# Kernel optimization log

Measured on AMD Instinct MI355X. Metric: run time of the kernel, lower is better.

Reference implementation:

```python
import math
import jax, jax.numpy as jnp
import numpy as np

B, T, S = 2, 2048, 2048
D_MODEL, N_HEADS = 1024, 16
HEAD_DIM = D_MODEL // N_HEADS
OUT_DIM = 1024


def setup_inputs() -> dict:
    key = jax.random.key(0)
    ks = jax.random.split(key, 6)
    q = jax.random.normal(ks[0], (B, T, D_MODEL), dtype=jnp.float32)
    k = jax.random.normal(ks[1], (B, S, D_MODEL), dtype=jnp.float32)
    v = jax.random.normal(ks[2], (B, S, D_MODEL), dtype=jnp.float32)
    rel_pos_bias = jax.random.normal(ks[3], (T, S, N_HEADS), dtype=jnp.float32)
    # shared qkv projection weight (torch ModuleList([Linear]*3) aliases one module)
    lim = 1.0 / math.sqrt(D_MODEL)
    Wqkv = jax.random.uniform(ks[4], (D_MODEL, D_MODEL), minval=-lim, maxval=lim, dtype=jnp.float32)
    Wout = jax.random.uniform(ks[5], (OUT_DIM, D_MODEL), minval=-lim, maxval=lim, dtype=jnp.float32)
    logit_scale = jnp.full((N_HEADS, 1, 1), math.log(10.0), dtype=jnp.float32)
    return {"q": q, "k": k, "v": v, "rel_pos_bias": rel_pos_bias,
            "Wqkv": Wqkv, "Wout": Wout, "logit_scale": logit_scale}


def _l2norm(x, eps=1e-12):
    # matches torch F.normalize(dim=-1)
    n = jnp.sqrt(jnp.sum(x * x, axis=-1, keepdims=True))
    return x / jnp.maximum(n, eps)


def reference(q, k, v, rel_pos_bias, Wqkv, Wout, logit_scale):
    # shared qkv projection (Linear, no bias): x @ W.T
    qp = q @ Wqkv.T
    kp = k @ Wqkv.T
    vp = v @ Wqkv.T
    # [B, H, T, Dh]
    qh = qp.reshape(B, T, N_HEADS, HEAD_DIM).transpose(0, 2, 1, 3)
    kh = kp.reshape(B, S, N_HEADS, HEAD_DIM).transpose(0, 2, 1, 3)
    vh = vp.reshape(B, S, N_HEADS, HEAD_DIM).transpose(0, 2, 1, 3)
    # cosine attention with clamped learned logit scale
    scale = jnp.exp(jnp.minimum(logit_scale, math.log(100.0)))  # [H,1,1]
    attn = jnp.einsum('bhtd,bhsd->bhts', _l2norm(qh), _l2norm(kh)) * scale
    # rel_pos_bias [T,S,H] -> [H,T,S], broadcast over batch
    attn = attn + rel_pos_bias.transpose(2, 0, 1)
    attn = jax.nn.softmax(attn, axis=-1)
    vals = jnp.einsum('bhts,bhsd->bhtd', attn, vh)
    vals = vals.transpose(0, 2, 1, 3).reshape(B, T, D_MODEL)
    return vals @ Wout.T
```

## Files before the change

### kernel.cpp

```cpp
#include <hip/hip_runtime.h>
#include <stdint.h>

typedef unsigned short u16;
using bf16x8 = __attribute__((ext_vector_type(8))) __bf16;
using f32x4  = __attribute__((ext_vector_type(4))) float;
using u16x8  = __attribute__((ext_vector_type(8))) u16;

#define BB 2
#define TT 2048
#define SQ 2048
#define DM 1024
#define NH 16
#define HD 64

__device__ __forceinline__ float bf2f(u16 u) {
  uint32_t x = ((uint32_t)u) << 16;
  return __builtin_bit_cast(float, x);
}
__device__ __forceinline__ u16 f2bf(float f) {
  uint32_t x = __builtin_bit_cast(uint32_t, f);
  x += 0x7fffu + ((x >> 16) & 1u);
  return (u16)(x >> 16);
}

typedef __attribute__((address_space(1))) void gvoid;
typedef __attribute__((address_space(3))) void lvoid;
__device__ __forceinline__ void g2l16(const void* g, void* l) {
  __builtin_amdgcn_global_load_lds((gvoid*)g, (lvoid*)l, 16, 0, 0);
}

__global__ __launch_bounds__(256) void convert_f32_bf16(
    const float* __restrict__ src, u16* __restrict__ dst, int n8) {
  int i = blockIdx.x * 256 + threadIdx.x;
  if (i >= n8) return;
  f32x4 a = ((const f32x4*)src)[(size_t)i * 2];
  f32x4 b = ((const f32x4*)src)[(size_t)i * 2 + 1];
  u16x8 o;
#pragma unroll
  for (int j = 0; j < 4; ++j) { o[j] = f2bf(a[j]); o[4 + j] = f2bf(b[j]); }
  ((u16x8*)dst)[i] = o;
}

template <typename OutT>
__device__ __forceinline__ void gemm_body(const u16* __restrict__ A,
                                          const u16* __restrict__ W,
                                          OutT* __restrict__ C,
                                          const float* __restrict__ ls,
                                          int norm_mode) {
  const int n0 = blockIdx.x * 128;
  const int m0 = blockIdx.y * 128;
  const int tid = threadIdx.x;
  const int w = tid >> 6, lane = tid & 63;
  const int l15 = lane & 15, lg = lane >> 4;
  const int wr = w >> 1, wc = w & 1;

  __shared__ u16 ldsA[16 * 512];
  __shared__ u16 ldsB[16 * 512];

  f32x4 acc[4][4];
#pragma unroll
  for (int i = 0; i < 4; ++i)
#pragma unroll
    for (int j = 0; j < 4; ++j) acc[i][j] = (f32x4){0.f, 0.f, 0.f, 0.f};

  for (int kt = 0; kt < 1024; kt += 64) {
#pragma unroll
    for (int u = 0; u < 4; ++u) {
      int f = w * 4 + u;
      int mt = f >> 1, ks = f & 1;
      g2l16(A + (size_t)(m0 + mt * 16 + l15) * 1024 + kt + ks * 32 + lg * 8,
            &ldsA[f * 512]);
      g2l16(W + (size_t)(n0 + mt * 16 + l15) * 1024 + kt + ks * 32 + lg * 8,
            &ldsB[f * 512]);
    }
    __syncthreads();
#pragma unroll
    for (int ks = 0; ks < 2; ++ks) {
      bf16x8 a[4], b[4];
#pragma unroll
      for (int i = 0; i < 4; ++i)
        a[i] = *(const bf16x8*)&ldsA[((wr * 4 + i) * 2 + ks) * 512 + lane * 8];
#pragma unroll
      for (int j = 0; j < 4; ++j)
        b[j] = *(const bf16x8*)&ldsB[((wc * 4 + j) * 2 + ks) * 512 + lane * 8];
#pragma unroll
      for (int i = 0; i < 4; ++i)
#pragma unroll
        for (int j = 0; j < 4; ++j)
          acc[i][j] = __builtin_amdgcn_mfma_f32_16x16x32_bf16(a[i], b[j],
                                                              acc[i][j], 0, 0, 0);
    }
    __syncthreads();
  }

  if (norm_mode < 2) {
    float sc = 1.0f;
    if (norm_mode == 0) sc = __expf(fminf(ls[(n0 >> 6) + wc], 4.60517019f));
#pragma unroll
    for (int i = 0; i < 4; ++i)
#pragma unroll
      for (int r = 0; r < 4; ++r) {
        float ss = 0.f;
#pragma unroll
        for (int j = 0; j < 4; ++j) ss += acc[i][j][r] * acc[i][j][r];
#pragma unroll
        for (int d = 1; d < 16; d <<= 1) ss += __shfl_xor(ss, d, 64);
        float f = sc / fmaxf(sqrtf(ss), 1e-12f);
#pragma unroll
        for (int j = 0; j < 4; ++j) acc[i][j][r] *= f;
      }
  }

#pragma unroll
  for (int i = 0; i < 4; ++i) {
    int row0 = m0 + (wr * 4 + i) * 16 + lg * 4;
#pragma unroll
    for (int j = 0; j < 4; ++j) {
      int col = n0 + (wc * 4 + j) * 16 + l15;
#pragma unroll
      for (int r = 0; r < 4; ++r) {
        if constexpr (sizeof(OutT) == 2)
          C[(size_t)(row0 + r) * 1024 + col] = f2bf(acc[i][j][r]);
        else
          C[(size_t)(row0 + r) * 1024 + col] = acc[i][j][r];
      }
    }
  }
}

__global__ __launch_bounds__(256, 2) void gemm_qkv(
    const u16* __restrict__ q, const u16* __restrict__ k,
    const u16* __restrict__ v, const u16* __restrict__ W,
    const float* __restrict__ ls,
    u16* __restrict__ qp, u16* __restrict__ kp, u16* __restrict__ vp) {
  const u16* A;
  u16* C;
  if (blockIdx.z == 0) { A = q; C = qp; }
  else if (blockIdx.z == 1) { A = k; C = kp; }
  else { A = v; C = vp; }
  gemm_body<u16>(A, W, C, ls, blockIdx.z);
}

__global__ __launch_bounds__(256, 2) void gemm_out(const u16* __restrict__ A,
                                                   const u16* __restrict__ W,
                                                   float* __restrict__ C) {
  gemm_body<float>(A, W, C, nullptr, 2);
}

__global__ __launch_bounds__(256) void transpose_v(const u16* __restrict__ vp,
                                                   u16* __restrict__ vt) {
  int st = blockIdx.x;
  int bh = blockIdx.y;
  __shared__ u16 lds[64][72];
  int tid = threadIdx.x;
  int s = tid >> 2, c0 = (tid & 3) * 16;
  int b = bh >> 4, h = bh & 15;
  const u16* src = vp + (size_t)(b * SQ + st * 64 + s) * 1024 + h * 64 + c0;
  u16x8 r0 = *(const u16x8*)src;
  u16x8 r1 = *(const u16x8*)(src + 8);
#pragma unroll
  for (int j = 0; j < 8; ++j) { lds[s][c0 + j] = r0[j]; lds[s][c0 + 8 + j] = r1[j]; }
  __syncthreads();
  int d = tid >> 2, sc = (tid & 3) * 16;
  u16x8 o0, o1;
#pragma unroll
  for (int j = 0; j < 8; ++j) { o0[j] = lds[sc + j][d]; o1[j] = lds[sc + 8 + j][d]; }
  u16* dst = vt + (size_t)(bh * 64 + d) * SQ + st * 64 + sc;
  *(u16x8*)dst = o0;
  *((u16x8*)(dst + 8)) = o1;
}

__global__ __launch_bounds__(256) void transpose_bias(const float* __restrict__ bias,
                                                      u16* __restrict__ bt) {
  int t = blockIdx.y;
  int s0 = blockIdx.x * 512;
  __shared__ u16 lds[16][520];
  int tid = threadIdx.x;
  const float* src = bias + ((size_t)t * SQ + s0 + tid * 2) * 16;
  float v[32];
#pragma unroll
  for (int j = 0; j < 8; ++j) {
    f32x4 r = ((const f32x4*)src)[j];
#pragma unroll
    for (int e = 0; e < 4; ++e) v[j * 4 + e] = r[e];
  }
  int sl = tid * 2;
#pragma unroll
  for (int e = 0; e < 32; ++e) lds[e & 15][sl + (e >> 4)] = f2bf(v[e]);
  __syncthreads();
  int h = tid >> 4, sc = (tid & 15) * 32;
  u16* dst = bt + ((size_t)h * TT + t) * SQ + s0 + sc;
#pragma unroll
  for (int j = 0; j < 4; ++j) {
    u16x8 o;
#pragma unroll
    for (int e = 0; e < 8; ++e) o[e] = lds[h][sc + j * 8 + e];
    *((u16x8*)(dst + j * 8)) = o;
  }
}

__global__ __launch_bounds__(256, 2) void flash_attn(
    const u16* __restrict__ qn, const u16* __restrict__ kn,
    const u16* __restrict__ vt, const u16* __restrict__ bt,
    u16* __restrict__ av) {
  const int h = blockIdx.x >> 1, b = blockIdx.x & 1, qt = blockIdx.y;
  const int tid = threadIdx.x, w = tid >> 6, lane = tid & 63;
  const int l15 = lane & 15, lg = lane >> 4;

  __shared__ u16 ldsK[16 * 512];
  __shared__ u16 ldsV[16 * 512];
  __shared__ u16 ldsP[4][16 * 136];

  const int t0 = qt * 64 + w * 16;

  bf16x8 qf[2];
  {
    const u16* qb = qn + (size_t)(b * TT + t0 + l15) * 1024 + h * 64 + lg * 8;
    qf[0] = *(const bf16x8*)qb;
    qf[1] = *(const bf16x8*)(qb + 32);
  }

  f32x4 o[4];
  float li[4];
#pragma unroll
  for (int r = 0; r < 4; ++r) li[r] = 0.f;
#pragma unroll
  for (int n = 0; n < 4; ++n) o[n] = (f32x4){0.f, 0.f, 0.f, 0.f};

  const u16* kb = kn + (size_t)(b * SQ) * 1024 + h * 64;
  const u16* vb = vt + (size_t)((b * NH + h) * 64) * SQ;
  const u16* bb = bt + ((size_t)h * TT + t0) * SQ;

  for (int st = 0; st < SQ; st += 128) {
#pragma unroll
    for (int u = 0; u < 4; ++u) {
      int f = w * 4 + u;
      int nt = f >> 1, ks = f & 1;
      g2l16(kb + (size_t)(st + nt * 16 + l15) * 1024 + ks * 32 + lg * 8,
            &ldsK[f * 512]);
      int j = f >> 2, ks2 = f & 3;
      g2l16(vb + (size_t)(j * 16 + l15) * SQ + st + ks2 * 32 + lg * 8,
            &ldsV[f * 512]);
    }

    float bv[8][4];
#pragma unroll
    for (int nt = 0; nt < 8; ++nt)
#pragma unroll
      for (int r = 0; r < 4; ++r)
        bv[nt][r] = bf2f(bb[(size_t)(lg * 4 + r) * SQ + st + nt * 16 + l15]);

    __syncthreads();

    f32x4 sacc[8];
#pragma unroll
    for (int nt = 0; nt < 8; ++nt) {
      sacc[nt] = (f32x4){0.f, 0.f, 0.f, 0.f};
#pragma unroll
      for (int ks = 0; ks < 2; ++ks)
        sacc[nt] = __builtin_amdgcn_mfma_f32_16x16x32_bf16(
            qf[ks], *(const bf16x8*)&ldsK[(nt * 2 + ks) * 512 + lane * 8],
            sacc[nt], 0, 0, 0);
    }

#pragma unroll
    for (int nt = 0; nt < 8; ++nt)
#pragma unroll
      for (int r = 0; r < 4; ++r) {
        float p = __expf(sacc[nt][r] + bv[nt][r]);
        li[r] += p;
        ldsP[w][(lg * 4 + r) * 136 + nt * 16 + l15] = f2bf(p);
      }

#pragma unroll
    for (int ks2 = 0; ks2 < 4; ++ks2) {
      bf16x8 pf = *(const bf16x8*)&ldsP[w][l15 * 136 + ks2 * 32 + lg * 8];
#pragma unroll
      for (int j = 0; j < 4; ++j)
        o[j] = __builtin_amdgcn_mfma_f32_16x16x32_bf16(
            pf, *(const bf16x8*)&ldsV[(j * 4 + ks2) * 512 + lane * 8], o[j],
            0, 0, 0);
    }
    __syncthreads();
  }

  float inv[4];
#pragma unroll
  for (int r = 0; r < 4; ++r) {
    float l = li[r];
#pragma unroll
    for (int d = 1; d < 16; d <<= 1) l += __shfl_xor(l, d, 64);
    inv[r] = 1.0f / l;
  }

#pragma unroll
  for (int j = 0; j < 4; ++j)
#pragma unroll
    for (int r = 0; r < 4; ++r) {
      size_t row = (size_t)(b * TT + t0 + lg * 4 + r);
      av[row * 1024 + h * 64 + j * 16 + l15] = f2bf(o[j][r] * inv[r]);
    }
}

extern "C" void kernel_launch(void* const* d_in, const int* in_sizes, int n_in,
                              void* d_out, int out_size, void* d_ws, size_t ws_size,
                              hipStream_t stream) {
  const float* q    = (const float*)d_in[0];
  const float* k    = (const float*)d_in[1];
  const float* v    = (const float*)d_in[2];
  const float* bias = (const float*)d_in[3];
  const float* Wqkv = (const float*)d_in[4];
  const float* Wout = (const float*)d_in[5];
  const float* ls   = (const float*)d_in[6];
  float* out = (float*)d_out;

  char* ws = (char*)d_ws;
  u16* qc = (u16*)(ws);
  u16* kc = (u16*)(ws + (size_t)(8  << 20));
  u16* vc = (u16*)(ws + (size_t)(16 << 20));
  u16* Wq = (u16*)(ws + (size_t)(24 << 20));
  u16* Wo = (u16*)(ws + (size_t)(26 << 20));
  u16* qn = (u16*)(ws + (size_t)(28 << 20));
  u16* kn = (u16*)(ws + (size_t)(36 << 20));
  u16* av = (u16*)(ws + (size_t)(44 << 20));
  u16* vtb = (u16*)(ws + (size_t)(52 << 20));
  u16* bt  = (u16*)(ws + (size_t)(60 << 20));

  dim3 blk(256);
  transpose_bias<<<dim3(4, 2048), blk, 0, stream>>>(bias, bt);
  convert_f32_bf16<<<dim3(2048), blk, 0, stream>>>(q, qc, 4096 * 1024 / 8);
  convert_f32_bf16<<<dim3(2048), blk, 0, stream>>>(k, kc, 4096 * 1024 / 8);
  convert_f32_bf16<<<dim3(2048), blk, 0, stream>>>(v, vc, 4096 * 1024 / 8);
  convert_f32_bf16<<<dim3(512),  blk, 0, stream>>>(Wqkv, Wq, 1024 * 1024 / 8);
  convert_f32_bf16<<<dim3(512),  blk, 0, stream>>>(Wout, Wo, 1024 * 1024 / 8);

  gemm_qkv<<<dim3(8, 32, 3), blk, 0, stream>>>(qc, kc, vc, Wq, ls, qn, kn, av);
  transpose_v<<<dim3(32, 32), blk, 0, stream>>>(av, vtb);
  flash_attn<<<dim3(32, 32), blk, 0, stream>>>(qn, kn, vtb, bt, av);
  gemm_out<<<dim3(8, 32), blk, 0, stream>>>(av, Wo, out);
}
```

Baseline: 642.1 us.

## Double-buffer K/V in flash attention, keep P in registers, fold log2e into scales

Flash attention now double-buffers K/V tiles in LDS, prefetching the next tile while computing on the current one with explicit vmcnt waits. Scores are computed transposed so P can be packed to bf16 and rearranged with permlane swaps, removing the LDS round trip for P. log2e is folded into the logit scale and the bias so the kernel can use exp2 directly, and the bias is loaded as vector u16x4 reads. The five conversion kernels are merged into one launch. This adds more LDS use and hand-tuned waitcnt logic that must stay correct.

```diff
diff --git a/kernel.cpp b/kernel.cpp
--- a/kernel.cpp
+++ b/kernel.cpp
@@ -5,6 +5,8 @@
 using bf16x8 = __attribute__((ext_vector_type(8))) __bf16;
 using f32x4  = __attribute__((ext_vector_type(4))) float;
 using u16x8  = __attribute__((ext_vector_type(8))) u16;
+using u16x4  = __attribute__((ext_vector_type(4))) u16;
+using i32x4  = __attribute__((ext_vector_type(4))) int;
 
 #define BB 2
 #define TT 2048
@@ -12,6 +14,7 @@
 #define DM 1024
 #define NH 16
 #define HD 64
+#define LOG2E 1.44269504088896340736f
 
 __device__ __forceinline__ float bf2f(u16 u) {
   uint32_t x = ((uint32_t)u) << 16;
@@ -22,6 +25,11 @@
   x += 0x7fffu + ((x >> 16) & 1u);
   return (u16)(x >> 16);
 }
+__device__ __forceinline__ int cvt_pk_bf16(float lo, float hi) {
+  int r;
+  asm("v_cvt_pk_bf16_f32 %0, %1, %2" : "=v"(r) : "v"(lo), "v"(hi));
+  return r;
+}
 
 typedef __attribute__((address_space(1))) void gvoid;
 typedef __attribute__((address_space(3))) void lvoid;
@@ -29,8 +37,21 @@
   __builtin_amdgcn_global_load_lds((gvoid*)g, (lvoid*)l, 16, 0, 0);
 }
 
-__global__ __launch_bounds__(256) void convert_f32_bf16(
-    const float* __restrict__ src, u16* __restrict__ dst, int n8) {
+__global__ __launch_bounds__(256) void convert_all(
+    const float* __restrict__ q, const float* __restrict__ k,
+    const float* __restrict__ v, const float* __restrict__ wq,
+    const float* __restrict__ wo, u16* __restrict__ qc, u16* __restrict__ kc,
+    u16* __restrict__ vc, u16* __restrict__ wqc, u16* __restrict__ woc) {
+  const float* src;
+  u16* dst;
+  int n8;
+  switch (blockIdx.y) {
+    case 0:  src = q;  dst = qc;  n8 = 4096 * 1024 / 8; break;
+    case 1:  src = k;  dst = kc;  n8 = 4096 * 1024 / 8; break;
+    case 2:  src = v;  dst = vc;  n8 = 4096 * 1024 / 8; break;
+    case 3:  src = wq; dst = wqc; n8 = 1024 * 1024 / 8; break;
+    default: src = wo; dst = woc; n8 = 1024 * 1024 / 8; break;
+  }
   int i = blockIdx.x * 256 + threadIdx.x;
   if (i >= n8) return;
   f32x4 a = ((const f32x4*)src)[(size_t)i * 2];
@@ -95,7 +116,8 @@
 
   if (norm_mode < 2) {
     float sc = 1.0f;
-    if (norm_mode == 0) sc = __expf(fminf(ls[(n0 >> 6) + wc], 4.60517019f));
+    if (norm_mode == 0)
+      sc = __expf(fminf(ls[(n0 >> 6) + wc], 4.60517019f)) * LOG2E;
 #pragma unroll
     for (int i = 0; i < 4; ++i)
 #pragma unroll
@@ -186,7 +208,7 @@
   }
   int sl = tid * 2;
 #pragma unroll
-  for (int e = 0; e < 32; ++e) lds[e & 15][sl + (e >> 4)] = f2bf(v[e]);
+  for (int e = 0; e < 32; ++e) lds[e & 15][sl + (e >> 4)] = f2bf(v[e] * LOG2E);
   __syncthreads();
   int h = tid >> 4, sc = (tid & 15) * 32;
   u16* dst = bt + ((size_t)h * TT + t) * SQ + s0 + sc;
@@ -207,9 +229,8 @@
   const int tid = threadIdx.x, w = tid >> 6, lane = tid & 63;
   const int l15 = lane & 15, lg = lane >> 4;
 
-  __shared__ u16 ldsK[16 * 512];
-  __shared__ u16 ldsV[16 * 512];
-  __shared__ u16 ldsP[4][16 * 136];
+  __shared__ u16 ldsK[2][16 * 512];
+  __shared__ u16 ldsV[2][16 * 512];
 
   const int t0 = qt * 64 + w * 16;
 
@@ -221,36 +242,46 @@
   }
 
   f32x4 o[4];
-  float li[4];
-#pragma unroll
-  for (int r = 0; r < 4; ++r) li[r] = 0.f;
 #pragma unroll
   for (int n = 0; n < 4; ++n) o[n] = (f32x4){0.f, 0.f, 0.f, 0.f};
+  float li = 0.f;
 
   const u16* kb = kn + (size_t)(b * SQ) * 1024 + h * 64;
   const u16* vb = vt + (size_t)((b * NH + h) * 64) * SQ;
-  const u16* bb = bt + ((size_t)h * TT + t0) * SQ;
-
-  for (int st = 0; st < SQ; st += 128) {
-#pragma unroll
-    for (int u = 0; u < 4; ++u) {
-      int f = w * 4 + u;
-      int nt = f >> 1, ks = f & 1;
-      g2l16(kb + (size_t)(st + nt * 16 + l15) * 1024 + ks * 32 + lg * 8,
-            &ldsK[f * 512]);
-      int j = f >> 2, ks2 = f & 3;
-      g2l16(vb + (size_t)(j * 16 + l15) * SQ + st + ks2 * 32 + lg * 8,
-            &ldsV[f * 512]);
-    }
-
-    float bv[8][4];
+  const u16* bbl = bt + ((size_t)h * TT + t0 + l15) * SQ + lg * 4;
+
+#define STAGE(bufi, stg)                                                       \
+  {                                                                            \
+    _Pragma("unroll") for (int u_ = 0; u_ < 4; ++u_) {                         \
+      int f_ = w * 4 + u_;                                                     \
+      int nt_ = f_ >> 1, ks_ = f_ & 1;                                         \
+      g2l16(kb + (size_t)((stg) + nt_ * 16 + l15) * 1024 + ks_ * 32 + lg * 8,  \
+            &ldsK[bufi][f_ * 512]);                                            \
+      int j_ = f_ >> 2, k2_ = f_ & 3;                                          \
+      g2l16(vb + (size_t)(j_ * 16 + l15) * SQ + (stg) + k2_ * 32 + lg * 8,     \
+            &ldsV[bufi][f_ * 512]);                                            \
+    }                                                                          \
+  }
+
+  STAGE(0, 0);
+
+  for (int it = 0; it < 16; ++it) {
+    const int cur = it & 1;
+    const int st = it * 128;
+
+    u16x4 bv[8];
 #pragma unroll
     for (int nt = 0; nt < 8; ++nt)
-#pragma unroll
-      for (int r = 0; r < 4; ++r)
-        bv[nt][r] = bf2f(bb[(size_t)(lg * 4 + r) * SQ + st + nt * 16 + l15]);
-
-    __syncthreads();
+      bv[nt] = *(const u16x4*)(bbl + st + nt * 16);
+    asm volatile("" ::: "memory");
+
+    if (it < 15) {
+      STAGE(cur ^ 1, st + 128);
+      asm volatile("s_waitcnt vmcnt(16)" ::: "memory");
+    } else {
+      asm volatile("s_waitcnt vmcnt(8)" ::: "memory");
+    }
+    __builtin_amdgcn_s_barrier();
 
     f32x4 sacc[8];
 #pragma unroll
@@ -259,39 +290,47 @@
 #pragma unroll
       for (int ks = 0; ks < 2; ++ks)
         sacc[nt] = __builtin_amdgcn_mfma_f32_16x16x32_bf16(
-            qf[ks], *(const bf16x8*)&ldsK[(nt * 2 + ks) * 512 + lane * 8],
-            sacc[nt], 0, 0, 0);
-    }
-
-#pragma unroll
-    for (int nt = 0; nt < 8; ++nt)
-#pragma unroll
-      for (int r = 0; r < 4; ++r) {
-        float p = __expf(sacc[nt][r] + bv[nt][r]);
-        li[r] += p;
-        ldsP[w][(lg * 4 + r) * 136 + nt * 16 + l15] = f2bf(p);
-      }
+            *(const bf16x8*)&ldsK[cur][(nt * 2 + ks) * 512 + lane * 8],
+            qf[ks], sacc[nt], 0, 0, 0);
+    }
+
+    int pk[8][2];
+#pragma unroll
+    for (int nt = 0; nt < 8; ++nt) {
+      float p0 = __builtin_amdgcn_exp2f(sacc[nt][0] + bf2f(bv[nt][0]));
+      float p1 = __builtin_amdgcn_exp2f(sacc[nt][1] + bf2f(bv[nt][1]));
+      float p2 = __builtin_amdgcn_exp2f(sacc[nt][2] + bf2f(bv[nt][2]));
+      float p3 = __builtin_amdgcn_exp2f(sacc[nt][3] + bf2f(bv[nt][3]));
+      li += (p0 + p1) + (p2 + p3);
+      pk[nt][0] = cvt_pk_bf16(p0, p1);
+      pk[nt][1] = cvt_pk_bf16(p2, p3);
+    }
 
 #pragma unroll
     for (int ks2 = 0; ks2 < 4; ++ks2) {
-      bf16x8 pf = *(const bf16x8*)&ldsP[w][l15 * 136 + ks2 * 32 + lg * 8];
+      auto a0 = __builtin_amdgcn_permlane32_swap(pk[2 * ks2][0],
+                                                 pk[2 * ks2 + 1][0], false, false);
+      auto w0 = __builtin_amdgcn_permlane16_swap(a0[0], a0[1], false, false);
+      auto a1 = __builtin_amdgcn_permlane32_swap(pk[2 * ks2][1],
+                                                 pk[2 * ks2 + 1][1], false, false);
+      auto w1 = __builtin_amdgcn_permlane16_swap(a1[0], a1[1], false, false);
+      i32x4 pw = (i32x4){(int)w0[0], (int)w1[0], (int)w0[1], (int)w1[1]};
+      bf16x8 pf = __builtin_bit_cast(bf16x8, pw);
 #pragma unroll
       for (int j = 0; j < 4; ++j)
         o[j] = __builtin_amdgcn_mfma_f32_16x16x32_bf16(
-            pf, *(const bf16x8*)&ldsV[(j * 4 + ks2) * 512 + lane * 8], o[j],
-            0, 0, 0);
-    }
-    __syncthreads();
-  }
-
+            pf, *(const bf16x8*)&ldsV[cur][(j * 4 + ks2) * 512 + lane * 8],
+            o[j], 0, 0, 0);
+    }
+    if (it < 15) __builtin_amdgcn_s_barrier();
+  }
+#undef STAGE
+
+  li += __shfl_xor(li, 16, 64);
+  li += __shfl_xor(li, 32, 64);
   float inv[4];
 #pragma unroll
-  for (int r = 0; r < 4; ++r) {
-    float l = li[r];
-#pragma unroll
-    for (int d = 1; d < 16; d <<= 1) l += __shfl_xor(l, d, 64);
-    inv[r] = 1.0f / l;
-  }
+  for (int r = 0; r < 4; ++r) inv[r] = 1.0f / __shfl(li, lg * 4 + r, 64);
 
 #pragma unroll
   for (int j = 0; j < 4; ++j)
@@ -328,11 +367,8 @@
 
   dim3 blk(256);
   transpose_bias<<<dim3(4, 2048), blk, 0, stream>>>(bias, bt);
-  convert_f32_bf16<<<dim3(2048), blk, 0, stream>>>(q, qc, 4096 * 1024 / 8);
-  convert_f32_bf16<<<dim3(2048), blk, 0, stream>>>(k, kc, 4096 * 1024 / 8);
-  convert_f32_bf16<<<dim3(2048), blk, 0, stream>>>(v, vc, 4096 * 1024 / 8);
-  convert_f32_bf16<<<dim3(512),  blk, 0, stream>>>(Wqkv, Wq, 1024 * 1024 / 8);
-  convert_f32_bf16<<<dim3(512),  blk, 0, stream>>>(Wout, Wo, 1024 * 1024 / 8);
+  convert_all<<<dim3(2048, 5), blk, 0, stream>>>(q, k, v, Wqkv, Wout,
+                                                 qc, kc, vc, Wq, Wo);
 
   gemm_qkv<<<dim3(8, 32, 3), blk, 0, stream>>>(qc, kc, vc, Wq, ls, qn, kn, av);
   transpose_v<<<dim3(32, 32), blk, 0, stream>>>(av, vtb);
```

Measured after the change: 650.1 us. About the same (+1.2%).
